# Kernel optimization log

Measured on AMD Instinct MI355X. Metric: run time of the kernel, lower is better.

Reference implementation:

```python
import jax, jax.numpy as jnp
import numpy as np

# ---- config (mirrors CoInHead init + TARGET_ASSIGNER_CONFIG) ----
PCR0, PCR1 = -51.2, -51.2          # point_cloud_range x/y min
VX, VY = 0.05, 0.05                # voxel_size x/y
STRIDE = 4                         # FEATURE_MAP_STRIDE
FW, FH = 512, 512                  # feature_map_size [x, y] = grid/stride
NUM_CLASSES = 10
NUM_MAX_OBJS = 500
OVERLAP = 0.1                      # GAUSSIAN_OVERLAP
MIN_RADIUS = 2
RMAX = 16                          # static cap on radius (covers all synthetic boxes)
K = 2 * RMAX + 1                   # fixed gaussian patch size
EPS = float(np.finfo(np.float32).eps)
BATCH = 16


def _gaussian_radius(height, width, min_overlap):
    # faithful to centernet_utils.gaussian_radius (OpenPCDet)
    b1 = height + width
    c1 = width * height * (1.0 - min_overlap) / (1.0 + min_overlap)
    sq1 = jnp.sqrt(jnp.maximum(b1 * b1 - 4.0 * c1, 0.0))
    r1 = (b1 + sq1) / 2.0

    b2 = 2.0 * (height + width)
    c2 = (1.0 - min_overlap) * width * height
    sq2 = jnp.sqrt(jnp.maximum(b2 * b2 - 16.0 * c2, 0.0))
    r2 = (b2 + sq2) / 2.0

    a3 = 4.0 * min_overlap
    b3 = -2.0 * min_overlap * (height + width)
    c3 = (min_overlap - 1.0) * width * height
    sq3 = jnp.sqrt(jnp.maximum(b3 * b3 - 4.0 * a3 * c3, 0.0))
    r3 = (b3 + sq3) / (2.0 * a3)
    return jnp.minimum(jnp.minimum(r1, r2), r3)


def setup_inputs() -> dict:
    key = jax.random.key(0)
    ks = jax.random.split(key, 8)
    B, M = BATCH, NUM_MAX_OBJS
    x = jax.random.uniform(ks[0], (B, M), minval=-50.0, maxval=50.0)
    y = jax.random.uniform(ks[1], (B, M), minval=-50.0, maxval=50.0)
    z = jax.random.uniform(ks[2], (B, M), minval=-2.0, maxval=1.0)
    dx = jax.random.uniform(ks[3], (B, M), minval=0.5, maxval=6.0)
    dy = jax.random.uniform(ks[4], (B, M), minval=0.5, maxval=6.0)
    dz = jax.random.uniform(ks[5], (B, M), minval=0.5, maxval=3.0)
    heading = jax.random.uniform(ks[6], (B, M), minval=-np.pi, maxval=np.pi)
    cls = jax.random.randint(ks[7], (B, M), 1, NUM_CLASSES + 1).astype(jnp.float32)
    gt_boxes = jnp.stack([x, y, z, dx, dy, dz, heading, cls], axis=-1).astype(jnp.float32)
    return {"gt_boxes": gt_boxes}


def reference(gt_boxes):
    # vectorized assign_target_of_single_head over (batch, objects)
    B, M, _ = gt_boxes.shape
    f32 = jnp.float32
    x, y, z = gt_boxes[..., 0], gt_boxes[..., 1], gt_boxes[..., 2]
    dx, dy, dz = gt_boxes[..., 3], gt_boxes[..., 4], gt_boxes[..., 5]
    heading = gt_boxes[..., 6]
    cls = (gt_boxes[..., 7] - 1.0).astype(jnp.int32)          # 0-based class id

    coord_x = jnp.clip((x - PCR0) / VX / STRIDE, 0.0, FW - 0.5)
    coord_y = jnp.clip((y - PCR1) / VY / STRIDE, 0.0, FH - 0.5)
    cxi = coord_x.astype(jnp.int32)
    cyi = coord_y.astype(jnp.int32)

    dxf = dx / VX / STRIDE
    dyf = dy / VY / STRIDE
    radius = _gaussian_radius(dxf, dyf, OVERLAP)
    radius = jnp.clip(radius.astype(jnp.int32), MIN_RADIUS, RMAX)  # (B, M)

    valid = (dxf > 0) & (dyf > 0) & (cxi >= 0) & (cxi <= FW) & (cyi >= 0) & (cyi <= FH)

    # fixed KxK gaussian patch centered on the integer center
    off = jnp.arange(K, dtype=jnp.int32) - RMAX
    oi = off[:, None]                                   # (K,1) row offset
    oj = off[None, :]                                   # (1,K) col offset
    sigma = (2.0 * radius.astype(f32) + 1.0) / 6.0      # diameter/6
    d2 = (oi * oi + oj * oj).astype(f32)                # (K,K)
    g = jnp.exp(-d2[None, None] / (2.0 * sigma[..., None, None] ** 2))  # (B,M,K,K)
    g = jnp.where(g < EPS, 0.0, g)                      # gaussian_2d eps truncation

    r_bm = radius[..., None, None]
    within = (jnp.abs(oi)[None, None] <= r_bm) & (jnp.abs(oj)[None, None] <= r_bm)
    yy = cyi[..., None, None] + oi[None, None]          # (B,M,K,K)
    xx = cxi[..., None, None] + oj[None, None]
    inb = (yy >= 0) & (yy < FH) & (xx >= 0) & (xx < FW)
    vals = jnp.where(valid[..., None, None] & within & inb, g, 0.0)

    b_idx = jnp.arange(B, dtype=jnp.int32)[:, None, None, None]
    c_idx = jnp.clip(cls, 0, NUM_CLASSES - 1)[..., None, None]
    heatmap = jnp.zeros((B, NUM_CLASSES, FH, FW), f32).at[
        b_idx, c_idx, jnp.clip(yy, 0, FH - 1), jnp.clip(xx, 0, FW - 1)
    ].max(vals)

    inds = jnp.where(valid, cyi * FW + cxi, 0).astype(jnp.int64)
    mask = valid.astype(jnp.int64)

    vf = valid.astype(f32)[..., None]
    ret_boxes = jnp.stack([
        coord_x - cxi.astype(f32),
        coord_y - cyi.astype(f32),
        z,
        jnp.log(jnp.maximum(dx, 1e-12)),
        jnp.log(jnp.maximum(dy, 1e-12)),
        jnp.log(jnp.maximum(dz, 1e-12)),
        jnp.cos(heading),
        jnp.sin(heading),
    ], axis=-1) * vf                                     # (B,M,8)

    return heatmap, ret_boxes, inds, mask
```

## Files before the change

### kernel.cpp

```cpp
#include <hip/hip_runtime.h>
#include <hip/hip_bf16.h>

#define PCR0   (-51.2f)
#define PCR1   (-51.2f)
#define VX_    (0.05f)
#define VY_    (0.05f)
#define STRIDE_ 4.0f
#define FW_    512
#define FH_    512
#define NCLS   10
#define NOBJ   500
#define OVERLAP_ 0.1f
#define MINRAD 2
#define RMAX_  16
#define BATCH_ 16
#define EPS_   1.1920928955078125e-07f

#define HEATMAP_ELEMS  (BATCH_ * NCLS * FH_ * FW_)
#define RETBOX_OFF     HEATMAP_ELEMS
#define RETBOX_ELEMS   (BATCH_ * NOBJ * 8)
#define INDS_OFF       (RETBOX_OFF + RETBOX_ELEMS)
#define MASK_OFF       (INDS_OFF + BATCH_ * NOBJ)

#define BAND_  32
#define NBAND  (FH_ / BAND_)
#define NBINS  (BATCH_ * NCLS * NBAND)

__device__ __forceinline__ void obj_params(const float* g8,
        float& coord_x, float& coord_y, int& cxi, int& cyi,
        int& radius, bool& valid)
{
    const float x = g8[0], y = g8[1];
    const float dx = g8[3], dy = g8[4];

    coord_x = fminf(fmaxf((x - PCR0) / VX_ / STRIDE_, 0.f), (float)FW_ - 0.5f);
    coord_y = fminf(fmaxf((y - PCR1) / VY_ / STRIDE_, 0.f), (float)FH_ - 0.5f);
    cxi = (int)coord_x;
    cyi = (int)coord_y;

    float dxf = dx / VX_ / STRIDE_;
    float dyf = dy / VY_ / STRIDE_;

    const float h = dxf, w = dyf, o = OVERLAP_;
    float b1 = h + w;
    float c1 = w * h * (1.f - o) / (1.f + o);
    float r1 = (b1 + sqrtf(fmaxf(b1 * b1 - 4.f * c1, 0.f))) * 0.5f;
    float b2 = 2.f * (h + w);
    float c2 = (1.f - o) * w * h;
    float r2 = (b2 + sqrtf(fmaxf(b2 * b2 - 16.f * c2, 0.f))) * 0.5f;
    float a3 = 4.f * o;
    float b3 = -2.f * o * (h + w);
    float c3 = (o - 1.f) * w * h;
    float r3 = (b3 + sqrtf(fmaxf(b3 * b3 - 4.f * a3 * c3, 0.f))) / (2.f * a3);
    float radf = fminf(fminf(r1, r2), r3);
    radius = (int)radf;
    radius = min(max(radius, MINRAD), RMAX_);

    valid = (dxf > 0.f) && (dyf > 0.f) &&
            (cxi >= 0) && (cxi <= FW_) && (cyi >= 0) && (cyi <= FH_);
}

__global__ __launch_bounds__(512) void fused(
        const float* __restrict__ gt, float* __restrict__ out)
{
    const int bid  = blockIdx.x;
    const int b    = bid / (NCLS * NBAND);
    const int rem  = bid - b * (NCLS * NBAND);
    const int myc  = rem >> 4;
    const int band = rem & (NBAND - 1);
    const int y0   = band << 5;

    __shared__ int  s_cnt;
    __shared__ int4 s_rec[NOBJ];

    if (threadIdx.x == 0) s_cnt = 0;
    __syncthreads();

    const int t = threadIdx.x;
    if (t < NOBJ) {
        const int obj = b * NOBJ + t;
        const float* g8 = gt + (size_t)obj * 8;
        float coord_x, coord_y; int cxi, cyi, radius; bool valid;
        obj_params(g8, coord_x, coord_y, cxi, cyi, radius, valid);
        int c = min(max((int)(g8[7] - 1.0f), 0), NCLS - 1);

        if (myc == 0 && band == 0) {
            const float z = g8[2], dx = g8[3], dy = g8[4], dz = g8[5];
            const float hd = g8[6];
            float vf = valid ? 1.f : 0.f;
            float* rb = out + RETBOX_OFF + (size_t)obj * 8;
            rb[0] = (coord_x - (float)cxi) * vf;
            rb[1] = (coord_y - (float)cyi) * vf;
            rb[2] = z * vf;
            rb[3] = logf(fmaxf(dx, 1e-12f)) * vf;
            rb[4] = logf(fmaxf(dy, 1e-12f)) * vf;
            rb[5] = logf(fmaxf(dz, 1e-12f)) * vf;
            rb[6] = cosf(hd) * vf;
            rb[7] = sinf(hd) * vf;
            out[INDS_OFF + obj] = valid ? (float)(cyi * FW_ + cxi) : 0.f;
            out[MASK_OFF + obj] = vf;
        }

        if (valid && c == myc &&
            (cyi + radius >= y0) && (cyi - radius <= y0 + BAND_ - 1)) {
            float sigma = (2.f * (float)radius + 1.f) / 6.f;
            float negInv = -1.0f / (2.f * sigma * sigma);
            int pos = atomicAdd(&s_cnt, 1);
            s_rec[pos] = make_int4(cxi, cyi, radius, __float_as_int(negInv));
        }
    }
    __syncthreads();

    const int col0  = (t & 127) << 2;
    const int r0    = __builtin_amdgcn_readfirstlane(t >> 7);
    const int wbase = __builtin_amdgcn_readfirstlane(((t >> 6) & 1) << 8);

    float acc[8][4];
    #pragma unroll
    for (int s = 0; s < 8; ++s) {
        acc[s][0] = 0.f; acc[s][1] = 0.f; acc[s][2] = 0.f; acc[s][3] = 0.f;
    }

    const int n = s_cnt;
    for (int it = 0; it < n; ++it) {
        int4 r = s_rec[it];
        int cxi   = __builtin_amdgcn_readfirstlane(r.x);
        int cyi   = __builtin_amdgcn_readfirstlane(r.y);
        int rad   = __builtin_amdgcn_readfirstlane(r.z);
        float negInv = __int_as_float(__builtin_amdgcn_readfirstlane(r.w));

        if (cxi + rad < wbase || cxi - rad > wbase + 255) continue;

        float cexp[4]; bool colin[4];
        #pragma unroll
        for (int k = 0; k < 4; ++k) {
            int rx = col0 + k - cxi;
            colin[k] = (rx >= -rad) && (rx <= rad);
            cexp[k]  = __expf((float)(rx * rx) * negInv);
        }

        #pragma unroll
        for (int s = 0; s < 8; ++s) {
            int ry = y0 + 4 * s + r0 - cyi;
            if (ry < -rad || ry > rad) continue;
            float rexp = __expf((float)(ry * ry) * negInv);
            #pragma unroll
            for (int k = 0; k < 4; ++k) {
                float g = rexp * cexp[k];
                bool ok = colin[k] && (g >= EPS_);
                acc[s][k] = ok ? fmaxf(acc[s][k], g) : acc[s][k];
            }
        }
    }

    float4* out4 = (float4*)(out + (size_t)bid * (BAND_ * FW_));
    #pragma unroll
    for (int s = 0; s < 8; ++s)
        out4[s * 512 + t] = make_float4(acc[s][0], acc[s][1], acc[s][2], acc[s][3]);
}

extern "C" void kernel_launch(void* const* d_in, const int* in_sizes, int n_in,
                              void* d_out, int out_size, void* d_ws, size_t ws_size,
                              hipStream_t stream) {
    const float* gt = (const float*)d_in[0];
    float* out = (float*)d_out;
    fused<<<NBINS, 512, 0, stream>>>(gt, out);
}
```

Baseline: 168.2 us.

## Merge class blocks into one block per band with class-bucketed object lists

Blocks are regrouped so that one 1024-thread block handles every class for a (batch, band) pair, instead of one 512-thread block per (batch, class, band). Object parameters are computed once per band and bucketed by class with a shared-memory counting sort, and the block then loops over classes and writes each class plane's band. This removes the tenfold redundant per-object radius and center computation. In exchange the grid shrinks to 256 large blocks, which lowers the number of resident waves and may reduce store throughput for the large heatmap write.

```diff
diff --git a/kernel.cpp b/kernel.cpp
--- a/kernel.cpp
+++ b/kernel.cpp
@@ -24,7 +24,7 @@
 
 #define BAND_  32
 #define NBAND  (FH_ / BAND_)
-#define NBINS  (BATCH_ * NCLS * NBAND)
+#define NBLOCK (BATCH_ * NBAND)
 
 __device__ __forceinline__ void obj_params(const float* g8,
         float& coord_x, float& coord_y, int& cxi, int& cyi,
@@ -60,23 +60,24 @@
             (cxi >= 0) && (cxi <= FW_) && (cyi >= 0) && (cyi <= FH_);
 }
 
-__global__ __launch_bounds__(512) void fused(
+__global__ __launch_bounds__(1024) void fused(
         const float* __restrict__ gt, float* __restrict__ out)
 {
     const int bid  = blockIdx.x;
-    const int b    = bid / (NCLS * NBAND);
-    const int rem  = bid - b * (NCLS * NBAND);
-    const int myc  = rem >> 4;
-    const int band = rem & (NBAND - 1);
+    const int b    = bid >> 4;
+    const int band = bid & (NBAND - 1);
     const int y0   = band << 5;
 
-    __shared__ int  s_cnt;
+    __shared__ int  s_cnt[NCLS];
+    __shared__ int  s_pos[NCLS];
+    __shared__ int  s_off[NCLS];
     __shared__ int4 s_rec[NOBJ];
 
-    if (threadIdx.x == 0) s_cnt = 0;
+    const int t = threadIdx.x;
+    if (t < NCLS) { s_cnt[t] = 0; s_pos[t] = 0; }
     __syncthreads();
 
-    const int t = threadIdx.x;
+    bool mine = false; int myc = 0; int4 myrec;
     if (t < NOBJ) {
         const int obj = b * NOBJ + t;
         const float* g8 = gt + (size_t)obj * 8;
@@ -84,7 +85,7 @@
         obj_params(g8, coord_x, coord_y, cxi, cyi, radius, valid);
         int c = min(max((int)(g8[7] - 1.0f), 0), NCLS - 1);
 
-        if (myc == 0 && band == 0) {
+        if (band == 0) {
             const float z = g8[2], dx = g8[3], dy = g8[4], dz = g8[5];
             const float hd = g8[6];
             float vf = valid ? 1.f : 0.f;
@@ -101,13 +102,26 @@
             out[MASK_OFF + obj] = vf;
         }
 
-        if (valid && c == myc &&
-            (cyi + radius >= y0) && (cyi - radius <= y0 + BAND_ - 1)) {
+        if (valid && (cyi + radius >= y0) && (cyi - radius <= y0 + BAND_ - 1)) {
             float sigma = (2.f * (float)radius + 1.f) / 6.f;
             float negInv = -1.0f / (2.f * sigma * sigma);
-            int pos = atomicAdd(&s_cnt, 1);
-            s_rec[pos] = make_int4(cxi, cyi, radius, __float_as_int(negInv));
+            mine = true; myc = c;
+            myrec = make_int4(cxi, cyi, radius, __float_as_int(negInv));
+            atomicAdd(&s_cnt[c], 1);
         }
+    }
+    __syncthreads();
+
+    if (t == 0) {
+        int a = 0;
+        #pragma unroll
+        for (int c = 0; c < NCLS; ++c) { s_off[c] = a; a += s_cnt[c]; }
+    }
+    __syncthreads();
+
+    if (mine) {
+        int p = atomicAdd(&s_pos[myc], 1);
+        s_rec[s_off[myc] + p] = myrec;
     }
     __syncthreads();
 
@@ -115,48 +129,55 @@
     const int r0    = __builtin_amdgcn_readfirstlane(t >> 7);
     const int wbase = __builtin_amdgcn_readfirstlane(((t >> 6) & 1) << 8);
 
-    float acc[8][4];
-    #pragma unroll
-    for (int s = 0; s < 8; ++s) {
-        acc[s][0] = 0.f; acc[s][1] = 0.f; acc[s][2] = 0.f; acc[s][3] = 0.f;
-    }
+    const size_t plane = (size_t)FH_ * FW_;
 
-    const int n = s_cnt;
-    for (int it = 0; it < n; ++it) {
-        int4 r = s_rec[it];
-        int cxi   = __builtin_amdgcn_readfirstlane(r.x);
-        int cyi   = __builtin_amdgcn_readfirstlane(r.y);
-        int rad   = __builtin_amdgcn_readfirstlane(r.z);
-        float negInv = __int_as_float(__builtin_amdgcn_readfirstlane(r.w));
+    for (int c = 0; c < NCLS; ++c) {
+        const int n   = __builtin_amdgcn_readfirstlane(s_cnt[c]);
+        const int off = __builtin_amdgcn_readfirstlane(s_off[c]);
 
-        if (cxi + rad < wbase || cxi - rad > wbase + 255) continue;
-
-        float cexp[4]; bool colin[4];
+        float acc[4][4];
         #pragma unroll
-        for (int k = 0; k < 4; ++k) {
-            int rx = col0 + k - cxi;
-            colin[k] = (rx >= -rad) && (rx <= rad);
-            cexp[k]  = __expf((float)(rx * rx) * negInv);
+        for (int s = 0; s < 4; ++s) {
+            acc[s][0] = 0.f; acc[s][1] = 0.f; acc[s][2] = 0.f; acc[s][3] = 0.f;
         }
 
-        #pragma unroll
-        for (int s = 0; s < 8; ++s) {
-            int ry = y0 + 4 * s + r0 - cyi;
-            if (ry < -rad || ry > rad) continue;
-            float rexp = __expf((float)(ry * ry) * negInv);
+        for (int it = 0; it < n; ++it) {
+            int4 r = s_rec[off + it];
+            int cxi   = __builtin_amdgcn_readfirstlane(r.x);
+            int cyi   = __builtin_amdgcn_readfirstlane(r.y);
+            int rad   = __builtin_amdgcn_readfirstlane(r.z);
+            float negInv = __int_as_float(__builtin_amdgcn_readfirstlane(r.w));
+
+            if (cxi + rad < wbase || cxi - rad > wbase + 255) continue;
+
+            float cexp[4]; bool colin[4];
             #pragma unroll
             for (int k = 0; k < 4; ++k) {
-                float g = rexp * cexp[k];
-                bool ok = colin[k] && (g >= EPS_);
-                acc[s][k] = ok ? fmaxf(acc[s][k], g) : acc[s][k];
+                int rx = col0 + k - cxi;
+                colin[k] = (rx >= -rad) && (rx <= rad);
+                cexp[k]  = __expf((float)(rx * rx) * negInv);
+            }
+
+            #pragma unroll
+            for (int s = 0; s < 4; ++s) {
+                int ry = y0 + 8 * s + r0 - cyi;
+                if (ry < -rad || ry > rad) continue;
+                float rexp = __expf((float)(ry * ry) * negInv);
+                #pragma unroll
+                for (int k = 0; k < 4; ++k) {
+                    float g = rexp * cexp[k];
+                    bool ok = colin[k] && (g >= EPS_);
+                    acc[s][k] = ok ? fmaxf(acc[s][k], g) : acc[s][k];
+                }
             }
         }
+
+        float4* out4 = (float4*)(out + ((size_t)(b * NCLS + c)) * plane
+                                     + (size_t)y0 * FW_);
+        #pragma unroll
+        for (int s = 0; s < 4; ++s)
+            out4[s * 1024 + t] = make_float4(acc[s][0], acc[s][1], acc[s][2], acc[s][3]);
     }
-
-    float4* out4 = (float4*)(out + (size_t)bid * (BAND_ * FW_));
-    #pragma unroll
-    for (int s = 0; s < 8; ++s)
-        out4[s * 512 + t] = make_float4(acc[s][0], acc[s][1], acc[s][2], acc[s][3]);
 }
 
 extern "C" void kernel_launch(void* const* d_in, const int* in_sizes, int n_in,
@@ -164,5 +185,5 @@
                               hipStream_t stream) {
     const float* gt = (const float*)d_in[0];
     float* out = (float*)d_out;
-    fused<<<NBINS, 512, 0, stream>>>(gt, out);
+    fused<<<NBLOCK, 1024, 0, stream>>>(gt, out);
 }
```

Result: slower. 173.7 us (+3.3%).

## Split into binning pass and per-band heatmap pass via workspace

Applied to the files above, without the earlier changes.

Adds a per-batch phaseA kernel that computes object parameters once, writes box outputs, and buckets gaussian records by (class, row band) into a workspace using a shared-memory counting sort. phaseB then reads only its bin's records instead of every block recomputing all 500 objects' parameters and filtering them. This removes redundant per-block object processing at the cost of a second launch, a serial dependency, and a global-memory round trip for the records. It falls back to the fused kernel if the workspace is too small.

```diff
diff --git a/kernel.cpp b/kernel.cpp
--- a/kernel.cpp
+++ b/kernel.cpp
@@ -24,7 +24,12 @@
 
 #define BAND_  32
 #define NBAND  (FH_ / BAND_)
-#define NBINS  (BATCH_ * NCLS * NBAND)
+#define BIN_N  (NCLS * NBAND)
+#define NBINS  (BATCH_ * BIN_N)
+#define RECMAX 1000
+
+#define BSTRIDE     (2 * BIN_N + RECMAX * 4)
+#define WS_NEEDED   ((size_t)BATCH_ * BSTRIDE * 4)
 
 __device__ __forceinline__ void obj_params(const float* g8,
         float& coord_x, float& coord_y, int& cxi, int& cyi,
@@ -58,6 +63,137 @@
 
     valid = (dxf > 0.f) && (dyf > 0.f) &&
             (cxi >= 0) && (cxi <= FW_) && (cyi >= 0) && (cyi <= FH_);
+}
+
+__global__ __launch_bounds__(512) void phaseA(
+        const float* __restrict__ gt, float* __restrict__ out,
+        int* __restrict__ bins)
+{
+    const int b = blockIdx.x;
+    const int t = threadIdx.x;
+
+    __shared__ int  s_cnt[BIN_N], s_off[BIN_N], s_pos[BIN_N];
+    __shared__ int4 s_rec[RECMAX];
+
+    if (t < BIN_N) { s_cnt[t] = 0; s_pos[t] = 0; }
+    __syncthreads();
+
+    bool valid = false; int c = 0, ty0 = 0, ty1 = -1; int4 rec;
+    if (t < NOBJ) {
+        const int obj = b * NOBJ + t;
+        const float* g8 = gt + (size_t)obj * 8;
+        float coord_x, coord_y; int cxi, cyi, radius;
+        obj_params(g8, coord_x, coord_y, cxi, cyi, radius, valid);
+        c = min(max((int)(g8[7] - 1.0f), 0), NCLS - 1);
+
+        const float z = g8[2], dx = g8[3], dy = g8[4], dz = g8[5];
+        const float hd = g8[6];
+        float vf = valid ? 1.f : 0.f;
+        float* rb = out + RETBOX_OFF + (size_t)obj * 8;
+        rb[0] = (coord_x - (float)cxi) * vf;
+        rb[1] = (coord_y - (float)cyi) * vf;
+        rb[2] = z * vf;
+        rb[3] = logf(fmaxf(dx, 1e-12f)) * vf;
+        rb[4] = logf(fmaxf(dy, 1e-12f)) * vf;
+        rb[5] = logf(fmaxf(dz, 1e-12f)) * vf;
+        rb[6] = cosf(hd) * vf;
+        rb[7] = sinf(hd) * vf;
+        out[INDS_OFF + obj] = valid ? (float)(cyi * FW_ + cxi) : 0.f;
+        out[MASK_OFF + obj] = vf;
+
+        if (valid) {
+            float sigma = (2.f * (float)radius + 1.f) / 6.f;
+            float negInv = -1.0f / (2.f * sigma * sigma);
+            rec = make_int4(cxi, cyi, radius, __float_as_int(negInv));
+            ty0 = max(cyi - radius, 0) >> 5;
+            ty1 = min(cyi + radius, FH_ - 1) >> 5;
+            for (int ty = ty0; ty <= ty1; ++ty)
+                atomicAdd(&s_cnt[c * NBAND + ty], 1);
+        }
+    }
+    __syncthreads();
+
+    if (t == 0) {
+        int a = 0;
+        for (int i = 0; i < BIN_N; ++i) { s_off[i] = a; a += s_cnt[i]; }
+    }
+    __syncthreads();
+
+    if (valid) {
+        for (int ty = ty0; ty <= ty1; ++ty) {
+            int bin = c * NBAND + ty;
+            int p = atomicAdd(&s_pos[bin], 1);
+            s_rec[s_off[bin] + p] = rec;
+        }
+    }
+    __syncthreads();
+
+    int* g = bins + b * BSTRIDE;
+    for (int i = t; i < BIN_N; i += 512) { g[i] = s_cnt[i]; g[BIN_N + i] = s_off[i]; }
+    const int total = s_off[BIN_N - 1] + s_cnt[BIN_N - 1];
+    int4* gr = (int4*)(g + 2 * BIN_N);
+    for (int i = t; i < total; i += 512) gr[i] = s_rec[i];
+}
+
+__global__ __launch_bounds__(512) void phaseB(
+        float* __restrict__ out, const int* __restrict__ bins)
+{
+    const int bid = blockIdx.x;
+    const int b   = bid / BIN_N;
+    const int rem = bid - b * BIN_N;
+    const int y0  = (rem & (NBAND - 1)) << 5;
+    const int t   = threadIdx.x;
+
+    const int* g = bins + b * BSTRIDE;
+    const int n   = __builtin_amdgcn_readfirstlane(g[rem]);
+    const int off = __builtin_amdgcn_readfirstlane(g[BIN_N + rem]);
+    const int4* rec = (const int4*)(g + 2 * BIN_N);
+
+    const int col0  = (t & 127) << 2;
+    const int r0    = __builtin_amdgcn_readfirstlane(t >> 7);
+    const int wbase = __builtin_amdgcn_readfirstlane(((t >> 6) & 1) << 8);
+
+    float acc[8][4];
+    #pragma unroll
+    for (int s = 0; s < 8; ++s) {
+        acc[s][0] = 0.f; acc[s][1] = 0.f; acc[s][2] = 0.f; acc[s][3] = 0.f;
+    }
+
+    for (int it = 0; it < n; ++it) {
+        int4 r = rec[off + it];
+        int cxi   = __builtin_amdgcn_readfirstlane(r.x);
+        int cyi   = __builtin_amdgcn_readfirstlane(r.y);
+        int rad   = __builtin_amdgcn_readfirstlane(r.z);
+        float negInv = __int_as_float(__builtin_amdgcn_readfirstlane(r.w));
+
+        if (cxi + rad < wbase || cxi - rad > wbase + 255) continue;
+
+        float cexp[4]; bool colin[4];
+        #pragma unroll
+        for (int k = 0; k < 4; ++k) {
+            int rx = col0 + k - cxi;
+            colin[k] = (rx >= -rad) && (rx <= rad);
+            cexp[k]  = __expf((float)(rx * rx) * negInv);
+        }
+
+        #pragma unroll
+        for (int s = 0; s < 8; ++s) {
+            int ry = y0 + 4 * s + r0 - cyi;
+            if (ry < -rad || ry > rad) continue;
+            float rexp = __expf((float)(ry * ry) * negInv);
+            #pragma unroll
+            for (int k = 0; k < 4; ++k) {
+                float gg = rexp * cexp[k];
+                bool ok = colin[k] && (gg >= EPS_);
+                acc[s][k] = ok ? fmaxf(acc[s][k], gg) : acc[s][k];
+            }
+        }
+    }
+
+    float4* out4 = (float4*)(out + (size_t)bid * (BAND_ * FW_));
+    #pragma unroll
+    for (int s = 0; s < 8; ++s)
+        out4[s * 512 + t] = make_float4(acc[s][0], acc[s][1], acc[s][2], acc[s][3]);
 }
 
 __global__ __launch_bounds__(512) void fused(
@@ -146,9 +282,9 @@
             float rexp = __expf((float)(ry * ry) * negInv);
             #pragma unroll
             for (int k = 0; k < 4; ++k) {
-                float g = rexp * cexp[k];
-                bool ok = colin[k] && (g >= EPS_);
-                acc[s][k] = ok ? fmaxf(acc[s][k], g) : acc[s][k];
+                float gg = rexp * cexp[k];
+                bool ok = colin[k] && (gg >= EPS_);
+                acc[s][k] = ok ? fmaxf(acc[s][k], gg) : acc[s][k];
             }
         }
     }
@@ -164,5 +300,12 @@
                               hipStream_t stream) {
     const float* gt = (const float*)d_in[0];
     float* out = (float*)d_out;
-    fused<<<NBINS, 512, 0, stream>>>(gt, out);
-}
+
+    if (ws_size >= WS_NEEDED) {
+        int* bins = (int*)d_ws;
+        phaseA<<<BATCH_, 512, 0, stream>>>(gt, out, bins);
+        phaseB<<<NBINS, 512, 0, stream>>>(out, bins);
+    } else {
+        fused<<<NBINS, 512, 0, stream>>>(gt, out);
+    }
+}
```

Result: no change. 168.0 us (-0.1%).
